# Kernel optimization log

Measured on AMD Instinct MI355X. Metric: run time of the kernel, lower is better.

Reference implementation:

```python
import jax, jax.numpy as jnp
import numpy as np

B, N, CIN, H, COUT = 256, 400, 128, 128, 16
THRESH = 0.6
EPS = 1e-5


def setup_inputs() -> dict:
    key = jax.random.key(0)
    ks = jax.random.split(key, 20)
    rn = lambda k, s, sc: jax.random.normal(k, s, jnp.float32) * sc
    inp = {
        "x": rn(ks[0], (B, N, CIN), 1.0),
        "adj": rn(ks[1], (B, N, N), 1.0),
        "edge": jax.random.randint(ks[2], (2, 4096), 0, N),  # unused (recomputed from adj in original)
        "batch": jnp.repeat(jnp.arange(B), N).reshape(B, N),  # graph ids; dense layout => mean over axis 1
        "W_adj": rn(ks[3], (N, N), 1.0 / np.sqrt(N)),
        "b_adj": rn(ks[4], (N,), 0.02),
        "W1": rn(ks[5], (CIN, H), 1.0 / np.sqrt(CIN)),
        "a_src1": rn(ks[6], (H,), 1.0 / np.sqrt(H)),
        "a_dst1": rn(ks[7], (H,), 1.0 / np.sqrt(H)),
        "b1": rn(ks[8], (H,), 0.02),
        "W2": rn(ks[9], (H, H), 1.0 / np.sqrt(H)),
        "a_src2": rn(ks[10], (H,), 1.0 / np.sqrt(H)),
        "a_dst2": rn(ks[11], (H,), 1.0 / np.sqrt(H)),
        "b2": rn(ks[12], (H,), 0.02),
        "ln_g": jnp.ones((H,), jnp.float32),
        "ln_b": jnp.zeros((H,), jnp.float32),
        "W_lin": rn(ks[13], (H, COUT), 1.0 / np.sqrt(H)),
        "b_lin": rn(ks[14], (COUT,), 0.02),
    }
    return inp


def _layer_norm(x, g, b):
    m = x.mean(-1, keepdims=True)
    v = ((x - m) ** 2).mean(-1, keepdims=True)
    return (x - m) * jax.lax.rsqrt(v + EPS) * g + b


def _gat(h, mask, W, a_src, a_dst, b):
    # PyG GATConv (1 head): edge i(src)->j(dst), softmax over incoming src nodes.
    hp = h @ W                                   # [B,N,H]
    e_src = hp @ a_src                           # [B,N]
    e_dst = hp @ a_dst                           # [B,N]
    score = jax.nn.leaky_relu(e_src[:, :, None] + e_dst[:, None, :], 0.2)  # [B,S,D]
    score = jnp.where(mask, score, jnp.finfo(score.dtype).min)
    alpha = jax.nn.softmax(score, axis=1)        # softmax over source axis per dst
    return jnp.einsum('bsd,bsh->bdh', alpha, hp) + b


def reference(x, adj, edge, batch, W_adj, b_adj, W1, a_src1, a_dst1, b1,
              W2, a_src2, a_dst2, b2, ln_g, ln_b, W_lin, b_lin):
    # adj -> Linear -> sigmoid -> detach -> threshold(0.6) -> binary edge mask
    a = jax.nn.sigmoid(adj @ W_adj + b_adj)
    mask = jax.lax.stop_gradient(a > THRESH)
    mask = mask | jnp.eye(N, dtype=bool)         # GATConv add_self_loops=True

    h = _gat(x, mask, W1, a_src1, a_dst1, b1)
    h = jax.nn.relu(_layer_norm(h, ln_g, ln_b))
    h = _gat(h, mask, W2, a_src2, a_dst2, b2)
    h = jax.nn.relu(_layer_norm(h, ln_g, ln_b))
    h = _gat(h, mask, W2, a_src2, a_dst2, b2)    # conv2 applied twice in original
    g = h.mean(axis=1)                           # global_mean_pool (dense per-graph layout)
    # dropout p=0.5 is identity in eval mode
    return g @ W_lin + b_lin                     # [B, COUT]
```

## Files before the change

kernel.cpp:

```cpp
#include <hip/hip_runtime.h>
#include <hip/hip_bf16.h>
#include <math.h>

#define NB 256
#define NN 400
#define NH 128
#define NCOUT 16
#define NNP 416
#define KP  416

static constexpr float LOGIT_THRESH = 0.40546510810816444f;
static constexpr float LN_EPS = 1e-5f;

typedef __attribute__((ext_vector_type(8))) short short8v;
typedef __attribute__((ext_vector_type(4))) float f32x4;

static __device__ __forceinline__ short f2bf_rne(float f) {
    unsigned u = __float_as_uint(f);
    unsigned r = (u + 0x7fff + ((u >> 16) & 1)) >> 16;
    return (short)r;
}
static __device__ __forceinline__ float bf2f(short s) {
    return __uint_as_float(((unsigned)(unsigned short)s) << 16);
}

static __device__ __forceinline__ unsigned pk_bf16(float a, float b) {
    __hip_bfloat162 h = __float22bfloat162_rn(make_float2(a, b));
    unsigned r;
    __builtin_memcpy(&r, &h, 4);
    return r;
}
static __device__ __forceinline__ void cvt8v(const float x[8], short8v& hv) {
    unsigned* hp = (unsigned*)&hv;
#pragma unroll
    for (int q = 0; q < 4; ++q) hp[q] = pk_bf16(x[2 * q], x[2 * q + 1]);
}

static __device__ __forceinline__ void gload16(const void* g, void* l) {
    __builtin_amdgcn_global_load_lds((const __attribute__((address_space(1))) void*)g,
                                     (__attribute__((address_space(3))) void*)l, 16, 0, 0);
}

__global__ __launch_bounds__(256) void k_wprep(const float* __restrict__ W,
                                               short* __restrict__ WtH)
{
    const int k0 = blockIdx.x * 32, d0 = blockIdx.y * 32;
    __shared__ float tile[32][33];
    const int t = threadIdx.x, cc = t & 31, rr = t >> 5;
#pragma unroll
    for (int i = 0; i < 4; ++i) {
        int k = k0 + rr + i * 8, d = d0 + cc;
        tile[rr + i * 8][cc] = (k < NN && d < NN) ? W[k * NN + d] : 0.f;
    }
    __syncthreads();
#pragma unroll
    for (int i = 0; i < 4; ++i) {
        int dr = rr + i * 8;
        int d = d0 + dr, k = k0 + cc;
        WtH[d * KP + k] = f2bf_rne(tile[cc][dr]);
    }
}

__global__ __launch_bounds__(256) void k_wprepW(const float* __restrict__ W,
                                                short* __restrict__ WTH)
{
    const int t = blockIdx.x * 256 + threadIdx.x;
    const int h = t >> 7, k = t & 127;
    WTH[h * NH + k] = f2bf_rne(W[k * NH + h]);
}

__global__ __launch_bounds__(256) void k_mask(const float* __restrict__ adj,
                                              const short* __restrict__ WtH,
                                              const float* __restrict__ badj,
                                              unsigned char* __restrict__ maskT)
{
    const int j   = blockIdx.x;
    const int xcd = j & 7;
    const int li  = j >> 3;
    const int panel  = xcd * 128 + (li >> 2);
    const int member = li & 3;
    const int b  = panel >> 2;
    const int s0 = (panel & 3) * 128;
    const int d0 = member * 128;

    const int t = threadIdx.x;
    const int lane = t & 63, w = t >> 6;
    const int wm = w >> 1, wn = w & 1;
    const int fr = lane & 15, fc = lane >> 4;

    __shared__ float As[2][128 * 32];
    __shared__ short Bhs[2][128 * 32];

    const float* adjb = adj + (long)b * NN * NN;

    long aG[4];
    int  aRow[4];
#pragma unroll
    for (int i = 0; i < 4; ++i) {
        int rloc = w * 32 + i * 8 + (lane >> 3);
        aRow[i] = rloc;
        int srow = s0 + rloc; srow = srow < NN ? srow : NN - 1;
        int c = (lane & 7) ^ (rloc & 7);
        aG[i] = (long)srow * NN + c * 4;
    }
    long bG[2];
#pragma unroll
    for (int i = 0; i < 2; ++i) {
        int rloc = w * 32 + i * 16 + (lane >> 2);
        int drow = d0 + rloc;
        int c = (lane & 3) ^ ((rloc >> 1) & 3);
        bG[i] = (long)drow * KP + c * 8;
    }

    f32x4 acc[4][4];
#pragma unroll
    for (int mi = 0; mi < 4; ++mi)
#pragma unroll
        for (int ni = 0; ni < 4; ++ni) acc[mi][ni] = (f32x4){0.f, 0.f, 0.f, 0.f};

    const int ca0 = (2 * fc) ^ (fr & 7);
    const int ca1 = (2 * fc + 1) ^ (fr & 7);
    const int cb  = fc ^ ((fr >> 1) & 3);

    #define STAGE(KT, BUF)                                                            \
    do {                                                                              \
        const int k0_ = (KT) * 32;                                                    \
        _Pragma("unroll")                                                             \
        for (int i = 0; i < 4; ++i) {                                                 \
            long gi = aG[i] + k0_;                                                    \
            if ((KT) == 12) {                                                         \
                int c = (lane & 7) ^ (aRow[i] & 7);                                   \
                if (c >= 4) gi = aG[i] - (long)c * 4;                                 \
            }                                                                         \
            gload16(adjb + gi, (char*)&As[BUF][0] + (w * 32 + i * 8) * 128);          \
        }                                                                             \
        _Pragma("unroll")                                                             \
        for (int i = 0; i < 2; ++i) {                                                 \
            gload16(WtH + bG[i] + k0_, (char*)&Bhs[BUF][0] + (w * 32 + i * 16) * 64); \
        }                                                                             \
    } while (0)

    STAGE(0, 0);
    asm volatile("s_waitcnt vmcnt(0)" ::: "memory");
    __builtin_amdgcn_s_barrier();

    int cur = 0;
    for (int kt = 0; kt < 13; ++kt) {
        __builtin_amdgcn_s_barrier();
        if (kt < 12) STAGE(kt + 1, cur ^ 1);
        if (kt < 12) asm volatile("s_waitcnt vmcnt(6)" ::: "memory");
        else         asm volatile("s_waitcnt vmcnt(0)" ::: "memory");
        __builtin_amdgcn_s_barrier();
        __builtin_amdgcn_sched_barrier(0);

        short8v ah[4], bh[4];
#pragma unroll
        for (int m = 0; m < 4; ++m) {
            const int row = wm * 64 + m * 16 + fr;
            float4 u0 = *(const float4*)((const char*)&As[cur][0] + row * 128 + ca0 * 16);
            float4 u1 = *(const float4*)((const char*)&As[cur][0] + row * 128 + ca1 * 16);
            float x[8] = {u0.x, u0.y, u0.z, u0.w, u1.x, u1.y, u1.z, u1.w};
            cvt8v(x, ah[m]);
        }
#pragma unroll
        for (int n = 0; n < 4; ++n) {
            const int row = wn * 64 + n * 16 + fr;
            bh[n] = *(const short8v*)((const char*)&Bhs[cur][0] + row * 64 + cb * 16);
        }
#pragma unroll
        for (int mi = 0; mi < 4; ++mi)
#pragma unroll
            for (int ni = 0; ni < 4; ++ni)
                acc[mi][ni] = __builtin_amdgcn_mfma_f32_16x16x32_bf16(ah[mi], bh[ni], acc[mi][ni], 0, 0, 0);
        cur ^= 1;
    }
    #undef STAGE

    unsigned char* mTb = maskT + (long)b * 32 * 52 * 128;
    const int dgbase = (d0 >> 4) + wn * 4;
    const int scbase = ((s0 + wm * 64) >> 3) + (fc >> 1);
    const int off8   = (fc & 1) * 4;
#pragma unroll
    for (int ni = 0; ni < 4; ++ni) {
        const int d = d0 + wn * 64 + ni * 16 + fr;
        if (d >= NN) continue;
        const float bv = badj[d];
#pragma unroll
        for (int mi = 0; mi < 4; ++mi) {
            const int s_cb = s0 + wm * 64 + mi * 16 + fc * 4;
            if (s_cb >= NNP) continue;
            uchar4 pk;
#pragma unroll
            for (int jj = 0; jj < 4; ++jj) {
                const int s = s_cb + jj;
                bool v = (s < NN) && ((acc[mi][ni][jj] + bv) > LOGIT_THRESH || s == d);
                ((unsigned char*)&pk)[jj] = v ? 1 : 0;
            }
            *(uchar4*)&mTb[((long)(dgbase + ni) * 52 + (scbase + mi * 2)) * 128 + fr * 8 + off8] = pk;
        }
    }
}

__global__ __launch_bounds__(256) void k_hp(const float* __restrict__ hin,
                                            const short* __restrict__ WTH,
                                            const float* __restrict__ asrc,
                                            const float* __restrict__ adst,
                                            short* __restrict__ hpT,
                                            float* __restrict__ e1sA, float* __restrict__ e2sA,
                                            float* __restrict__ e1dA, float* __restrict__ e2dA)
{
    const int b  = blockIdx.y;
    const int s0 = blockIdx.x * 128;
    const int t  = threadIdx.x;
    const int lane = t & 63, w = t >> 6;
    const int wm = w >> 1, wn = w & 1;
    const int fr = lane & 15, fc = lane >> 4;

    const float* hb = hin + (long)b * NN * NH;
    short* hpTb = hpT + (long)b * NH * NNP;

    f32x4 acc[4][4];
#pragma unroll
    for (int m = 0; m < 4; ++m)
#pragma unroll
        for (int n = 0; n < 4; ++n) acc[m][n] = (f32x4){0.f, 0.f, 0.f, 0.f};

    for (int kt = 0; kt < 4; ++kt) {
        const int k0 = kt * 32;
        short8v ah[4], bh[4];
#pragma unroll
        for (int m = 0; m < 4; ++m) {
            const int h = wm * 64 + m * 16 + fr;
            ah[m] = *(const short8v*)&WTH[h * NH + k0 + fc * 8];
        }
#pragma unroll
        for (int n = 0; n < 4; ++n) {
            const int s = s0 + wn * 64 + n * 16 + fr;
            float x[8];
            if (s < NN) {
                float4 u0 = *(const float4*)&hb[(long)s * NH + k0 + fc * 8];
                float4 u1 = *(const float4*)&hb[(long)s * NH + k0 + fc * 8 + 4];
                x[0]=u0.x; x[1]=u0.y; x[2]=u0.z; x[3]=u0.w;
                x[4]=u1.x; x[5]=u1.y; x[6]=u1.z; x[7]=u1.w;
            } else {
#pragma unroll
                for (int jj = 0; jj < 8; ++jj) x[jj] = 0.f;
            }
            cvt8v(x, bh[n]);
        }
#pragma unroll
        for (int m = 0; m < 4; ++m)
#pragma unroll
            for (int n = 0; n < 4; ++n)
                acc[m][n] = __builtin_amdgcn_mfma_f32_16x16x32_bf16(ah[m], bh[n], acc[m][n], 0, 0, 0);
    }

#pragma unroll
    for (int m = 0; m < 4; ++m) {
#pragma unroll
        for (int n = 0; n < 4; ++n) {
            const int s = s0 + wn * 64 + n * 16 + fr;
            if (s >= NNP) continue;
#pragma unroll
            for (int jj = 0; jj < 4; ++jj) {
                const int h = wm * 64 + m * 16 + fc * 4 + jj;
                hpTb[h * NNP + s] = f2bf_rne(acc[m][n][jj]);
            }
        }
    }

    __shared__ float esp[2][128], edp[2][128];
    float asv[4][4], adv[4][4];
#pragma unroll
    for (int m = 0; m < 4; ++m)
#pragma unroll
        for (int jj = 0; jj < 4; ++jj) {
            const int h = wm * 64 + m * 16 + fc * 4 + jj;
            asv[m][jj] = asrc[h];
            adv[m][jj] = adst[h];
        }
    float ps[4] = {0.f, 0.f, 0.f, 0.f}, pd[4] = {0.f, 0.f, 0.f, 0.f};
#pragma unroll
    for (int n = 0; n < 4; ++n)
#pragma unroll
        for (int m = 0; m < 4; ++m)
#pragma unroll
            for (int jj = 0; jj < 4; ++jj) {
                ps[n] += acc[m][n][jj] * asv[m][jj];
                pd[n] += acc[m][n][jj] * adv[m][jj];
            }
#pragma unroll
    for (int n = 0; n < 4; ++n) {
        ps[n] += __shfl_xor(ps[n], 16); ps[n] += __shfl_xor(ps[n], 32);
        pd[n] += __shfl_xor(pd[n], 16); pd[n] += __shfl_xor(pd[n], 32);
    }
    if (fc == 0) {
#pragma unroll
        for (int n = 0; n < 4; ++n) {
            esp[wm][wn * 64 + n * 16 + fr] = ps[n];
            edp[wm][wn * 64 + n * 16 + fr] = pd[n];
        }
    }
    __syncthreads();
    if (t < 128) {
        const int s = s0 + t;
        if (s < NNP) {
            const float es = esp[0][t] + esp[1][t];
            const float ed = edp[0][t] + edp[1][t];
            const long o = (long)b * NNP + s;
            e1sA[o] = __expf(es);       e2sA[o] = __expf(0.2f * es);
            e1dA[o] = __expf(ed);       e2dA[o] = __expf(0.2f * ed);
        }
    }
}

template<int DO_LN>
__global__ __launch_bounds__(256) void k_aggr(const unsigned char* __restrict__ maskT,
                                              const short* __restrict__ hpT,
                                              const float* __restrict__ e1sA,
                                              const float* __restrict__ e2sA,
                                              const float* __restrict__ e1dA,
                                              const float* __restrict__ e2dA,
                                              const float* __restrict__ bias,
                                              const float* __restrict__ lng,
                                              const float* __restrict__ lnb,
                                              float* __restrict__ hout)
{
    const int b  = blockIdx.y;
    const int d0 = blockIdx.x * 128;
    const int t  = threadIdx.x;
    const int lane = t & 63, w = t >> 6;
    const int wm = w >> 1, wn = w & 1;
    const int fr = lane & 15, fc = lane >> 4;

    __shared__ float e1s_l[NNP], e2s_l[NNP];
    __shared__ float den_l[128];
    __shared__ float lngl[128], lnbl[128];

    for (int i = t; i < NNP; i += 256) {
        const long o = (long)b * NNP + i;
        e1s_l[i] = e1sA[o];
        e2s_l[i] = e2sA[o];
    }
    if (DO_LN && t < 128) { lngl[t] = lng[t]; lnbl[t] = lnb[t]; }

    float e1dv[4], e2dv[4];
#pragma unroll
    for (int m = 0; m < 4; ++m) {
        const int d = d0 + wm * 64 + m * 16 + fr;
        const bool v = d < NN;
        const long o = (long)b * NNP + (v ? d : 0);
        e1dv[m] = v ? e1dA[o] : 0.f;
        e2dv[m] = v ? e2dA[o] : 0.f;
    }
    __syncthreads();

    f32x4 acc[4][4];
#pragma unroll
    for (int m = 0; m < 4; ++m)
#pragma unroll
        for (int n = 0; n < 4; ++n) acc[m][n] = (f32x4){0.f, 0.f, 0.f, 0.f};
    float den[4] = {0.f, 0.f, 0.f, 0.f};

    const unsigned char* mbase = maskT + (((long)b * 32 + (d0 >> 4) + wm * 4) * 52) * 128 + fr * 8;
    const short* hTb = hpT + (long)b * NH * NNP;

    for (int kt = 0; kt < 13; ++kt) {
        const int sb = kt * 32 + fc * 8;
        short8v bf_[4];
#pragma unroll
        for (int n = 0; n < 4; ++n) {
            const int h = wn * 64 + n * 16 + fr;
            bf_[n] = *(const short8v*)&hTb[h * NNP + sb];
        }
        float4 e1a = *(const float4*)&e1s_l[sb];
        float4 e1b = *(const float4*)&e1s_l[sb + 4];
        float4 e2a = *(const float4*)&e2s_l[sb];
        float4 e2b = *(const float4*)&e2s_l[sb + 4];
        float e18[8] = {e1a.x, e1a.y, e1a.z, e1a.w, e1b.x, e1b.y, e1b.z, e1b.w};
        float e28[8] = {e2a.x, e2a.y, e2a.z, e2a.w, e2b.x, e2b.y, e2b.z, e2b.w};
        const long scoff = (long)(kt * 4 + fc) * 128;
#pragma unroll
        for (int m = 0; m < 4; ++m) {
            const unsigned long long mk = *(const unsigned long long*)(mbase + (long)m * 52 * 128 + scoff);
            short8v pv;
            unsigned* pw = (unsigned*)&pv;
#pragma unroll
            for (int q = 0; q < 4; ++q) {
                float p0 = fmaxf(e18[2 * q] * e1dv[m],     e28[2 * q] * e2dv[m]);
                float p1 = fmaxf(e18[2 * q + 1] * e1dv[m], e28[2 * q + 1] * e2dv[m]);
                p0 = ((mk >> (16 * q)) & 0xffULL)     ? p0 : 0.f;
                p1 = ((mk >> (16 * q + 8)) & 0xffULL) ? p1 : 0.f;
                den[m] += p0 + p1;
                pw[q] = pk_bf16(p0, p1);
            }
#pragma unroll
            for (int n = 0; n < 4; ++n)
                acc[m][n] = __builtin_amdgcn_mfma_f32_16x16x32_bf16(pv, bf_[n], acc[m][n], 0, 0, 0);
        }
    }

#pragma unroll
    for (int m = 0; m < 4; ++m) {
        den[m] += __shfl_xor(den[m], 16);
        den[m] += __shfl_xor(den[m], 32);
    }
    if (wn == 0 && fc == 0) {
#pragma unroll
        for (int m = 0; m < 4; ++m) den_l[wm * 64 + m * 16 + fr] = den[m];
    }
    __syncthreads();

    float bvh[4];
#pragma unroll
    for (int n = 0; n < 4; ++n) bvh[n] = bias[wn * 64 + n * 16 + fr];

    float* hb = hout + (long)b * NN * NH;

    if (DO_LN) {
        __shared__ float Cm[32][132];
        for (int m = 0; m < 4; ++m) {
#pragma unroll
            for (int jj = 0; jj < 4; ++jj) {
                const int dl = wm * 64 + m * 16 + fc * 4 + jj;
                const float idn = 1.f / den_l[dl];
                const int r = wm * 16 + fc * 4 + jj;
#pragma unroll
                for (int n = 0; n < 4; ++n)
                    Cm[r][wn * 64 + n * 16 + fr] = acc[m][n][jj] * idn + bvh[n];
            }
            __syncthreads();
            {
                const int r = t >> 3, seg = t & 7;
                float s1 = 0.f, s2 = 0.f;
#pragma unroll
                for (int q = 0; q < 16; q += 4) {
                    float4 v = *(float4*)&Cm[r][seg * 16 + q];
                    s1 += v.x + v.y + v.z + v.w;
                    s2 += v.x * v.x + v.y * v.y + v.z * v.z + v.w * v.w;
                }
                s1 += __shfl_xor(s1, 1); s2 += __shfl_xor(s2, 1);
                s1 += __shfl_xor(s1, 2); s2 += __shfl_xor(s2, 2);
                s1 += __shfl_xor(s1, 4); s2 += __shfl_xor(s2, 4);
                const float mean = s1 * (1.f / 128.f);
                const float var  = s2 * (1.f / 128.f) - mean * mean;
                const float inv  = rsqrtf(fmaxf(var, 0.f) + LN_EPS);
                const int d = d0 + (r >> 4) * 64 + m * 16 + (r & 15);
                if (d < NN) {
                    float* po = hb + (long)d * NH;
#pragma unroll
                    for (int q = 0; q < 16; q += 4) {
                        const int cl = seg * 16 + q;
                        float4 v = *(float4*)&Cm[r][cl];
                        float4 o;
                        o.x = fmaxf((v.x - mean) * inv * lngl[cl]     + lnbl[cl],     0.f);
                        o.y = fmaxf((v.y - mean) * inv * lngl[cl + 1] + lnbl[cl + 1], 0.f);
                        o.z = fmaxf((v.z - mean) * inv * lngl[cl + 2] + lnbl[cl + 2], 0.f);
                        o.w = fmaxf((v.w - mean) * inv * lngl[cl + 3] + lnbl[cl + 3], 0.f);
                        *(float4*)&po[cl] = o;
                    }
                }
            }
            __syncthreads();
        }
    } else {
#pragma unroll
        for (int m = 0; m < 4; ++m) {
#pragma unroll
            for (int jj = 0; jj < 4; ++jj) {
                const int dl = wm * 64 + m * 16 + fc * 4 + jj;
                const int d = d0 + dl;
                if (d >= NN) continue;
                const float idn = 1.f / den_l[dl];
#pragma unroll
                for (int n = 0; n < 4; ++n) {
                    const int h = wn * 64 + n * 16 + fr;
                    hb[(long)d * NH + h] = acc[m][n][jj] * idn + bvh[n];
                }
            }
        }
    }
}

__global__ __launch_bounds__(128) void k_pool_lin(const float* __restrict__ h,
                                                  const float* __restrict__ Wl,
                                                  const float* __restrict__ bl,
                                                  float* __restrict__ out)
{
    const int b = blockIdx.x;
    const int t = threadIdx.x;
    const float* hb = h + (long)b * NN * NH;
    float s = 0.f;
    for (int n = 0; n < NN; ++n) s += hb[(long)n * NH + t];
    __shared__ float gl[128];
    gl[t] = s * (1.f / NN);
    __syncthreads();
    if (t < NCOUT) {
        float o = bl[t];
        for (int k = 0; k < NH; ++k) o += gl[k] * Wl[k * NCOUT + t];
        out[b * NCOUT + t] = o;
    }
}

extern "C" void kernel_launch(void* const* d_in, const int* in_sizes, int n_in,
                              void* d_out, int out_size, void* d_ws, size_t ws_size,
                              hipStream_t stream)
{
    const float* x    = (const float*)d_in[0];
    const float* adj  = (const float*)d_in[1];
    const float* Wadj = (const float*)d_in[4];
    const float* badj = (const float*)d_in[5];
    const float* W1   = (const float*)d_in[6];
    const float* as1  = (const float*)d_in[7];
    const float* ad1  = (const float*)d_in[8];
    const float* b1   = (const float*)d_in[9];
    const float* W2   = (const float*)d_in[10];
    const float* as2  = (const float*)d_in[11];
    const float* ad2  = (const float*)d_in[12];
    const float* b2   = (const float*)d_in[13];
    const float* lng  = (const float*)d_in[14];
    const float* lnb  = (const float*)d_in[15];
    const float* Wlin = (const float*)d_in[16];
    const float* blin = (const float*)d_in[17];
    float* out = (float*)d_out;

    char* ws = (char*)d_ws;
    unsigned char* maskT = (unsigned char*)ws;
    short* hpT  = (short*)(ws + 54525952);
    float* hbuf = (float*)(ws + 81788928);
    float* e1sA = (float*)(ws + 134217728);
    float* e2sA = (float*)(ws + 134643712);
    float* e1dA = (float*)(ws + 135069696);
    float* e2dA = (float*)(ws + 135495680);
    short* WtH  = (short*)(ws + 135921664);
    short* WT1H = (short*)(ws + 136347648);
    short* WT2H = (short*)(ws + 136380416);

    k_wprep<<<dim3(13, 16), dim3(256), 0, stream>>>(Wadj, WtH);
    k_wprepW<<<dim3(64), dim3(256), 0, stream>>>(W1, WT1H);
    k_wprepW<<<dim3(64), dim3(256), 0, stream>>>(W2, WT2H);
    k_mask<<<dim3(4096), dim3(256), 0, stream>>>(adj, WtH, badj, maskT);

    k_hp<<<dim3(4, NB), dim3(256), 0, stream>>>(x, WT1H, as1, ad1, hpT,
                                                e1sA, e2sA, e1dA, e2dA);
    k_aggr<1><<<dim3(4, NB), dim3(256), 0, stream>>>(maskT, hpT, e1sA, e2sA, e1dA, e2dA,
                                                     b1, lng, lnb, hbuf);

    k_hp<<<dim3(4, NB), dim3(256), 0, stream>>>(hbuf, WT2H, as2, ad2, hpT,
                                                e1sA, e2sA, e1dA, e2dA);
    k_aggr<1><<<dim3(4, NB), dim3(256), 0, stream>>>(maskT, hpT, e1sA, e2sA, e1dA, e2dA,
                                                     b2, lng, lnb, hbuf);

    k_hp<<<dim3(4, NB), dim3(256), 0, stream>>>(hbuf, WT2H, as2, ad2, hpT,
                                                e1sA, e2sA, e1dA, e2dA);
    k_aggr<0><<<dim3(4, NB), dim3(256), 0, stream>>>(maskT, hpT, e1sA, e2sA, e1dA, e2dA,
                                                     b2, lng, lnb, hbuf);

    k_pool_lin<<<dim3(NB), dim3(128), 0, stream>>>(hbuf, Wlin, blin, out);
}
```

Baseline: 412.1 us.

## Give each wave a full-width 32x128 output tile and fuse LayerNorm in registers

Each aggregation wave now owns 32 destination rows across all 128 hidden columns, instead of a 64x64 quadrant. Score/mask computation per destination row is therefore no longer duplicated across two waves, and LayerNorm row statistics can be reduced with lane shuffles in registers. This removes the shared-memory staging buffer and its per-m-block barriers. In exchange each wave loads twice as many hp B-fragments per k-step, and the epilogue writes use scalar strided stores instead of float4.

```diff
diff --git a/kernel.cpp b/kernel.cpp
--- a/kernel.cpp
+++ b/kernel.cpp
@@ -330,7 +330,6 @@
     const int d0 = blockIdx.x * 128;
     const int t  = threadIdx.x;
     const int lane = t & 63, w = t >> 6;
-    const int wm = w >> 1, wn = w & 1;
     const int fr = lane & 15, fc = lane >> 4;
 
     __shared__ float e1s_l[NNP], e2s_l[NNP];
@@ -344,10 +343,10 @@
     }
     if (DO_LN && t < 128) { lngl[t] = lng[t]; lnbl[t] = lnb[t]; }
 
-    float e1dv[4], e2dv[4];
-#pragma unroll
-    for (int m = 0; m < 4; ++m) {
-        const int d = d0 + wm * 64 + m * 16 + fr;
+    float e1dv[2], e2dv[2];
+#pragma unroll
+    for (int m = 0; m < 2; ++m) {
+        const int d = d0 + w * 32 + m * 16 + fr;
         const bool v = d < NN;
         const long o = (long)b * NNP + (v ? d : 0);
         e1dv[m] = v ? e1dA[o] : 0.f;
@@ -355,24 +354,22 @@
     }
     __syncthreads();
 
-    f32x4 acc[4][4];
-#pragma unroll
-    for (int m = 0; m < 4; ++m)
-#pragma unroll
-        for (int n = 0; n < 4; ++n) acc[m][n] = (f32x4){0.f, 0.f, 0.f, 0.f};
-    float den[4] = {0.f, 0.f, 0.f, 0.f};
-
-    const unsigned char* mbase = maskT + (((long)b * 32 + (d0 >> 4) + wm * 4) * 52) * 128 + fr * 8;
+    f32x4 acc[2][8];
+#pragma unroll
+    for (int m = 0; m < 2; ++m)
+#pragma unroll
+        for (int n = 0; n < 8; ++n) acc[m][n] = (f32x4){0.f, 0.f, 0.f, 0.f};
+    float den[2] = {0.f, 0.f};
+
+    const unsigned char* mbase = maskT + (((long)b * 32 + (d0 >> 4) + w * 2) * 52) * 128 + fr * 8;
     const short* hTb = hpT + (long)b * NH * NNP;
 
     for (int kt = 0; kt < 13; ++kt) {
         const int sb = kt * 32 + fc * 8;
-        short8v bf_[4];
-#pragma unroll
-        for (int n = 0; n < 4; ++n) {
-            const int h = wn * 64 + n * 16 + fr;
-            bf_[n] = *(const short8v*)&hTb[h * NNP + sb];
-        }
+        short8v bf_[8];
+#pragma unroll
+        for (int n = 0; n < 8; ++n)
+            bf_[n] = *(const short8v*)&hTb[(n * 16 + fr) * NNP + sb];
         float4 e1a = *(const float4*)&e1s_l[sb];
         float4 e1b = *(const float4*)&e1s_l[sb + 4];
         float4 e2a = *(const float4*)&e2s_l[sb];
@@ -381,7 +378,7 @@
         float e28[8] = {e2a.x, e2a.y, e2a.z, e2a.w, e2b.x, e2b.y, e2b.z, e2b.w};
         const long scoff = (long)(kt * 4 + fc) * 128;
 #pragma unroll
-        for (int m = 0; m < 4; ++m) {
+        for (int m = 0; m < 2; ++m) {
             const unsigned long long mk = *(const unsigned long long*)(mbase + (long)m * 52 * 128 + scoff);
             short8v pv;
             unsigned* pw = (unsigned*)&pv;
@@ -395,87 +392,66 @@
                 pw[q] = pk_bf16(p0, p1);
             }
 #pragma unroll
-            for (int n = 0; n < 4; ++n)
+            for (int n = 0; n < 8; ++n)
                 acc[m][n] = __builtin_amdgcn_mfma_f32_16x16x32_bf16(pv, bf_[n], acc[m][n], 0, 0, 0);
         }
     }
 
 #pragma unroll
-    for (int m = 0; m < 4; ++m) {
+    for (int m = 0; m < 2; ++m) {
         den[m] += __shfl_xor(den[m], 16);
         den[m] += __shfl_xor(den[m], 32);
     }
-    if (wn == 0 && fc == 0) {
-#pragma unroll
-        for (int m = 0; m < 4; ++m) den_l[wm * 64 + m * 16 + fr] = den[m];
+    if (fc == 0) {
+#pragma unroll
+        for (int m = 0; m < 2; ++m) den_l[w * 32 + m * 16 + fr] = den[m];
     }
     __syncthreads();
 
-    float bvh[4];
-#pragma unroll
-    for (int n = 0; n < 4; ++n) bvh[n] = bias[wn * 64 + n * 16 + fr];
+    float bvh[8], lgv[8], lbv[8];
+#pragma unroll
+    for (int n = 0; n < 8; ++n) {
+        bvh[n] = bias[n * 16 + fr];
+        if (DO_LN) { lgv[n] = lngl[n * 16 + fr]; lbv[n] = lnbl[n * 16 + fr]; }
+    }
 
     float* hb = hout + (long)b * NN * NH;
 
-    if (DO_LN) {
-        __shared__ float Cm[32][132];
-        for (int m = 0; m < 4; ++m) {
-#pragma unroll
-            for (int jj = 0; jj < 4; ++jj) {
-                const int dl = wm * 64 + m * 16 + fc * 4 + jj;
-                const float idn = 1.f / den_l[dl];
-                const int r = wm * 16 + fc * 4 + jj;
-#pragma unroll
-                for (int n = 0; n < 4; ++n)
-                    Cm[r][wn * 64 + n * 16 + fr] = acc[m][n][jj] * idn + bvh[n];
-            }
-            __syncthreads();
-            {
-                const int r = t >> 3, seg = t & 7;
+#pragma unroll
+    for (int m = 0; m < 2; ++m) {
+#pragma unroll
+        for (int jj = 0; jj < 4; ++jj) {
+            const int dl = w * 32 + m * 16 + fc * 4 + jj;
+            const int d = d0 + dl;
+            const float idn = 1.f / den_l[dl];
+            float v[8];
+            if (DO_LN) {
                 float s1 = 0.f, s2 = 0.f;
 #pragma unroll
-                for (int q = 0; q < 16; q += 4) {
-                    float4 v = *(float4*)&Cm[r][seg * 16 + q];
-                    s1 += v.x + v.y + v.z + v.w;
-                    s2 += v.x * v.x + v.y * v.y + v.z * v.z + v.w * v.w;
+                for (int n = 0; n < 8; ++n) {
+                    v[n] = acc[m][n][jj] * idn + bvh[n];
+                    s1 += v[n];
+                    s2 += v[n] * v[n];
                 }
                 s1 += __shfl_xor(s1, 1); s2 += __shfl_xor(s2, 1);
                 s1 += __shfl_xor(s1, 2); s2 += __shfl_xor(s2, 2);
                 s1 += __shfl_xor(s1, 4); s2 += __shfl_xor(s2, 4);
+                s1 += __shfl_xor(s1, 8); s2 += __shfl_xor(s2, 8);
                 const float mean = s1 * (1.f / 128.f);
                 const float var  = s2 * (1.f / 128.f) - mean * mean;
                 const float inv  = rsqrtf(fmaxf(var, 0.f) + LN_EPS);
-                const int d = d0 + (r >> 4) * 64 + m * 16 + (r & 15);
                 if (d < NN) {
                     float* po = hb + (long)d * NH;
 #pragma unroll
-                    for (int q = 0; q < 16; q += 4) {
-                        const int cl = seg * 16 + q;
-                        float4 v = *(float4*)&Cm[r][cl];
-                        float4 o;
-                        o.x = fmaxf((v.x - mean) * inv * lngl[cl]     + lnbl[cl],     0.f);
-                        o.y = fmaxf((v.y - mean) * inv * lngl[cl + 1] + lnbl[cl + 1], 0.f);
-                        o.z = fmaxf((v.z - mean) * inv * lngl[cl + 2] + lnbl[cl + 2], 0.f);
-                        o.w = fmaxf((v.w - mean) * inv * lngl[cl + 3] + lnbl[cl + 3], 0.f);
-                        *(float4*)&po[cl] = o;
-                    }
+                    for (int n = 0; n < 8; ++n)
+                        po[n * 16 + fr] = fmaxf((v[n] - mean) * inv * lgv[n] + lbv[n], 0.f);
                 }
-            }
-            __syncthreads();
-        }
-    } else {
-#pragma unroll
-        for (int m = 0; m < 4; ++m) {
-#pragma unroll
-            for (int jj = 0; jj < 4; ++jj) {
-                const int dl = wm * 64 + m * 16 + fc * 4 + jj;
-                const int d = d0 + dl;
-                if (d >= NN) continue;
-                const float idn = 1.f / den_l[dl];
-#pragma unroll
-                for (int n = 0; n < 4; ++n) {
-                    const int h = wn * 64 + n * 16 + fr;
-                    hb[(long)d * NH + h] = acc[m][n][jj] * idn + bvh[n];
+            } else {
+                if (d < NN) {
+                    float* po = hb + (long)d * NH;
+#pragma unroll
+                    for (int n = 0; n < 8; ++n)
+                        po[n * 16 + fr] = acc[m][n][jj] * idn + bvh[n];
                 }
             }
         }
```

Result: faster. 392.7 us (-4.7%).
